# Performance work log

Hardware: AMD Instinct MI355X
Metric: run time of the kernel (lower is better)

The kernel has to match this reference:

```python
import jax, jax.numpy as jnp
import numpy as np

P_SZ = 16      # patch size
N_PATCH = 196  # (224/16)^2
D = 768        # feat dim (= 3*16*16)
H = 3072       # mlp hidden
T = 8          # num task vectors
P_BLOCKS = 6   # param blocks: Wp, bp, W1, b1, W2, b2
META_H = 192   # max(768//4, T*P_BLOCKS)


def patchify(x):
    # x: [B,3,224,224] -> [B,196,768]
    B = x.shape[0]
    x = x.reshape(B, 3, 14, P_SZ, 14, P_SZ)
    x = x.transpose(0, 2, 4, 1, 3, 5)
    return x.reshape(B, N_PATCH, 3 * P_SZ * P_SZ)


def func0(params, xp):
    # surrogate linearized backbone on ONE sample's patches xp: [196,768] -> [768]
    Wp, bp, W1, b1, W2, b2 = params
    h = xp @ Wp + bp              # [196,768]
    f = h.mean(axis=0)            # [768]
    f = jax.nn.relu(f @ W1 + b1)  # [3072]
    return f @ W2 + b2            # [768]


def setup_inputs() -> dict:
    key = jax.random.key(0)
    ks = jax.random.split(key, 20)
    B = 32
    d = {}
    d['x'] = jax.random.normal(ks[0], (B, 3, 224, 224), dtype=jnp.float32)
    # base params0 (6 blocks)
    d['Wp'] = jax.random.normal(ks[1], (D, D), dtype=jnp.float32) * 0.02
    d['bp'] = jnp.zeros((D,), dtype=jnp.float32)
    d['W1'] = jax.random.normal(ks[2], (D, H), dtype=jnp.float32) * 0.02
    d['b1'] = jnp.zeros((H,), dtype=jnp.float32)
    d['W2'] = jax.random.normal(ks[3], (H, D), dtype=jnp.float32) * 0.02
    d['b2'] = jnp.zeros((D,), dtype=jnp.float32)
    # T stacked task-vector deltas, one per param block
    d['dWp'] = jax.random.normal(ks[4], (T, D, D), dtype=jnp.float32) * 0.01
    d['dbp'] = jax.random.normal(ks[5], (T, D), dtype=jnp.float32) * 0.01
    d['dW1'] = jax.random.normal(ks[6], (T, D, H), dtype=jnp.float32) * 0.01
    d['db1'] = jax.random.normal(ks[7], (T, H), dtype=jnp.float32) * 0.01
    d['dW2'] = jax.random.normal(ks[8], (T, H, D), dtype=jnp.float32) * 0.01
    d['db2'] = jax.random.normal(ks[9], (T, D), dtype=jnp.float32) * 0.01
    # MetaNet (Linear-ReLU-Linear), blockwise output T*P_BLOCKS
    d['mW1'] = jax.random.normal(ks[10], (D, META_H), dtype=jnp.float32) * 0.01
    d['mb1'] = jax.random.normal(ks[11], (META_H,), dtype=jnp.float32) * 0.01
    d['mW2'] = jax.random.normal(ks[12], (META_H, T * P_BLOCKS), dtype=jnp.float32) * 0.02
    d['mb2'] = jnp.zeros((T * P_BLOCKS,), dtype=jnp.float32)
    return d


def reference(x, Wp, bp, W1, b1, W2, b2,
              dWp, dbp, dW1, db1, dW2, db2,
              mW1, mb1, mW2, mb2):
    params0 = (Wp, bp, W1, b1, W2, b2)
    patches = patchify(x)                                  # [B,196,768]
    # base features (no grad in original)
    base_feat = jax.lax.stop_gradient(jax.vmap(lambda xp: func0(params0, xp))(patches))  # [B,768]
    # blockwise coefficients [B, T, P_BLOCKS]
    coefs = (jax.nn.relu(base_feat @ mW1 + mb1) @ mW2 + mb2).reshape(-1, T, P_BLOCKS)
    # batched weighted sum over task vectors, per parameter block
    dWp_b = jnp.einsum('bt,tij->bij', coefs[:, :, 0], dWp)
    dbp_b = jnp.einsum('bt,tj->bj',  coefs[:, :, 1], dbp)
    dW1_b = jnp.einsum('bt,tij->bij', coefs[:, :, 2], dW1)
    db1_b = jnp.einsum('bt,tj->bj',  coefs[:, :, 3], db1)
    dW2_b = jnp.einsum('bt,tij->bij', coefs[:, :, 4], dW2)
    db2_b = jnp.einsum('bt,tj->bj',  coefs[:, :, 5], db2)

    def single(xp, dp):
        out, dout = jax.jvp(lambda p: func0(p, xp), (params0,), (dp,))
        return out + dout

    outputs = jax.vmap(single)(patches, (dWp_b, dbp_b, dW1_b, db1_b, dW2_b, db2_b))
    return outputs  # [B,768]
```

## Files before the change

### kernel.cpp

```cpp
#include <hip/hip_runtime.h>


__global__ void patch_partial_k(const float* __restrict__ x, float* __restrict__ part) {
    int blk = blockIdx.x;
    int i  = blk % 14;
    int ch = (blk / 14) % 3;
    int b  = blk / 42;
    int t  = threadIdx.x;
    int py = t >> 4, px = t & 15;
    const float* xp = x + (((size_t)(b*3 + ch))*224 + (size_t)(i*16 + py))*224 + px;
    float s = 0.f;
#pragma unroll
    for (int j = 0; j < 14; ++j) s += xp[j*16];
    part[(size_t)blk*256 + t] = s;
}

__global__ void patch_reduce_k(const float* __restrict__ part, float* __restrict__ xbarT) {
    int idx = blockIdx.x*256 + threadIdx.x;
    int b = idx / 768;
    int c = idx % 768;
    int ch = c >> 8, t = c & 255;
    const float* p = part + ((size_t)(b*42 + ch*14))*256 + t;
    float s = 0.f;
#pragma unroll
    for (int i = 0; i < 14; ++i) s += p[i*256];
    xbarT[(size_t)c*32 + b] = s * (1.f/196.f);
}

#define LOADB(BUF)                                                   \
    _Pragma("unroll")                                                \
    for (int u = 0; u < 16; ++u) BUF[u] = bp[(size_t)u*N];           \
    bp += (size_t)16*N;

#define FMAC8(AR, BV)                                                \
    _Pragma("unroll")                                                \
    for (int m = 0; m < 8; ++m) {                                    \
        acc[4*m]   += AR[m].x * (BV);                                \
        acc[4*m+1] += AR[m].y * (BV);                                \
        acc[4*m+2] += AR[m].z * (BV);                                \
        acc[4*m+3] += AR[m].w * (BV);                                \
    }

#define PREF(AR, KIDX)                                               \
    _Pragma("unroll")                                                \
    for (int r = 0; r < 8; ++r)                                      \
        AR[r] = *(const float4*)(As + (KIDX)*32 + r*4);

#define HALF(BUF, KK)                                                \
    _Pragma("unroll")                                                \
    for (int u = 0; u < 16; u += 2) {                                \
        PREF(a1, (KK)+u+1)                                           \
        FMAC8(a0, BUF[u])                                            \
        PREF(a0, (KK)+u+2)                                           \
        FMAC8(a1, BUF[u+1])                                          \
    }

template<int N, int KW>
__global__ __launch_bounds__(256, 3) void gemm4_k(const float* __restrict__ AT,
                                                  const float* __restrict__ Bm,
                                                  float* __restrict__ P) {
    constexpr int KB = 4*KW;
    __shared__ float lds[8704];
    const int tid  = threadIdx.x;
    const int lane = tid & 63;
    const int wave = __builtin_amdgcn_readfirstlane(tid >> 6);
    const int col  = blockIdx.x*64 + lane;
    const size_t kblk = (size_t)blockIdx.y * KB;

    {
        const float4* Ag = (const float4*)(AT + kblk*32);
        float4* As4 = (float4*)lds;
#pragma unroll
        for (int i = 0; i < KB*32/4/256; ++i)
            As4[i*256 + tid] = Ag[i*256 + tid];
    }

    const float* bp = Bm + (kblk + (size_t)wave*KW)*N + col;
    float bvA[16], bvB[16];
    LOADB(bvA)

    __syncthreads();
    const float* As = lds + wave*KW*32;

    float acc[32];
#pragma unroll
    for (int m = 0; m < 32; ++m) acc[m] = 0.f;

    float4 a0[8], a1[8];
    PREF(a0, 0)

    if constexpr (KW == 16) {
        HALF(bvA, 0)
    } else {
#pragma unroll 1
        for (int kk = 0; kk + 32 <= KW; kk += 32) {
            LOADB(bvB)
            HALF(bvA, kk)
            if (kk + 32 < KW) { LOADB(bvA) }
            HALF(bvB, kk + 16)
        }
    }

    __syncthreads();
    {
        float* w0 = lds + (wave*64 + lane)*34;
#pragma unroll
        for (int m = 0; m < 32; m += 2)
            *(float2*)(w0 + m) = make_float2(acc[m], acc[m+1]);
    }
    __syncthreads();
    {
        const int c  = tid >> 2;
        const int mb = (tid & 3) * 8;
        float s[8];
#pragma unroll
        for (int j = 0; j < 8; j += 2) {
            float2 v0 = *(const float2*)(lds + (0*64 + c)*34 + mb + j);
            float2 v1 = *(const float2*)(lds + (1*64 + c)*34 + mb + j);
            float2 v2 = *(const float2*)(lds + (2*64 + c)*34 + mb + j);
            float2 v3 = *(const float2*)(lds + (3*64 + c)*34 + mb + j);
            s[j]   = v0.x + v1.x + v2.x + v3.x;
            s[j+1] = v0.y + v1.y + v2.y + v3.y;
        }
        float* p0 = P + (size_t)blockIdx.y*((size_t)N*32)
                      + ((size_t)blockIdx.x*64 + c)*32 + mb;
        *(float4*)(p0)     = make_float4(s[0], s[1], s[2], s[3]);
        *(float4*)(p0 + 4) = make_float4(s[4], s[5], s[6], s[7]);
    }
}

template<int Y>
__global__ void reduce_bias_k(const float* __restrict__ P, const float* __restrict__ bias,
                              float* __restrict__ out, int SZ) {
    int idx = blockIdx.x*256 + threadIdx.x;
    float s = bias[idx >> 5];
#pragma unroll
    for (int y = 0; y < Y; ++y) s += P[(size_t)y*SZ + idx];
    out[idx] = s;
}

template<int Y>
__global__ void reduce_zf_k(const float* __restrict__ P, const float* __restrict__ bias,
                            float* __restrict__ zT, float* __restrict__ fT) {
    int idx = blockIdx.x*256 + threadIdx.x;
    float s = bias[idx >> 5];
#pragma unroll
    for (int y = 0; y < Y; ++y) s += P[(size_t)y*98304 + idx];
    zT[idx] = s;
    fT[idx] = fmaxf(s, 0.f);
}

template<int Y>
__global__ void reduce_arr_k(const float* __restrict__ P, const float* __restrict__ init,
                             float* __restrict__ out, int SZ) {
    int idx = blockIdx.x*256 + threadIdx.x;
    float s = init[idx];
#pragma unroll
    for (int y = 0; y < Y; ++y) s += P[(size_t)y*SZ + idx];
    out[idx] = s;
}

template<int Y>
__global__ void reduce_mask_k(const float* __restrict__ P, const float* __restrict__ init,
                              const float* __restrict__ zT, float* __restrict__ dfT) {
    int idx = blockIdx.x*256 + threadIdx.x;
    float s = init[idx];
#pragma unroll 15
    for (int y = 0; y < Y; ++y) s += P[(size_t)y*98304 + idx];
    dfT[idx] = zT[idx] > 0.f ? s : 0.f;
}

template<int Y>
__global__ void reduce_out_k(const float* __restrict__ P, const float* __restrict__ init,
                             const float* __restrict__ baseT, float* __restrict__ out) {
    int idx = blockIdx.x*256 + threadIdx.x;
    float s = init[idx] + baseT[idx];
#pragma unroll 15
    for (int y = 0; y < Y; ++y) s += P[(size_t)y*24576 + idx];
    int n = idx >> 5, b = idx & 31;
    out[b*768 + n] = s;
}

__global__ void metanet1_k(const float* __restrict__ baseT, const float* __restrict__ mW1,
                           const float* __restrict__ mb1, float* __restrict__ v) {
    int b  = blockIdx.x;
    int jg = blockIdx.y;
    int jj = threadIdx.x & 31;
    int ks = threadIdx.x >> 5;
    int j  = jg*32 + jj;
    const float* wp = mW1 + (size_t)(ks*96)*192 + j;
    const float* xp = baseT + (size_t)(ks*96)*32 + b;
    float s = 0.f;
#pragma unroll 8
    for (int i = 0; i < 96; ++i) s += xp[i*32] * wp[i*192];
    __shared__ float red[256];
    red[threadIdx.x] = s;
    __syncthreads();
    if (threadIdx.x < 32) {
        float t = mb1[j];
#pragma unroll
        for (int k = 0; k < 8; ++k) t += red[k*32 + threadIdx.x];
        v[b*192 + jg*32 + threadIdx.x] = fmaxf(t, 0.f);
    }
}

__global__ void metanet2_k(const float* __restrict__ v, const float* __restrict__ mW2,
                           const float* __restrict__ mb2, float* __restrict__ coefs) {
    int b  = blockIdx.x;
    int o  = threadIdx.x & 63;
    int ks = threadIdx.x >> 6;
    float s = 0.f;
    if (o < 48) {
        const float* vp = v + b*192 + ks*48;
        const float* wp = mW2 + (size_t)(ks*48)*48 + o;
#pragma unroll 8
        for (int i = 0; i < 48; ++i) s += vp[i] * wp[i*48];
    }
    __shared__ float red[256];
    red[threadIdx.x] = s;
    __syncthreads();
    if (threadIdx.x < 48) {
        float t = mb2[threadIdx.x];
#pragma unroll
        for (int k = 0; k < 4; ++k) t += red[k*64 + threadIdx.x];
        coefs[b*48 + threadIdx.x] = t;
    }
}

__global__ void build_all_k(const float* __restrict__ coefs, const float* __restrict__ xbarT,
                            const float* __restrict__ f0T, const float* __restrict__ fT,
                            const float* __restrict__ dbp, const float* __restrict__ db1,
                            const float* __restrict__ db2,
                            float* __restrict__ G0T, float* __restrict__ G1T,
                            float* __restrict__ G2T, float* __restrict__ df0b,
                            float* __restrict__ dzb, float* __restrict__ doutb) {
    int idx = blockIdx.x*256 + threadIdx.x;
    int b = idx & 31;
    int r = idx >> 5;
    if (r < 6144) {
        int t = r / 768, i = r % 768;
        G0T[idx] = coefs[b*48 + t*6 + 0] * xbarT[(size_t)i*32 + b];
    } else if (r < 12288) {
        int rr = r - 6144;
        int t = rr / 768, i = rr % 768;
        G1T[(size_t)rr*32 + b] = coefs[b*48 + t*6 + 2] * f0T[(size_t)i*32 + b];
    } else if (r < 36864) {
        int rr = r - 12288;
        int t = rr / 3072, i = rr % 3072;
        G2T[(size_t)rr*32 + b] = coefs[b*48 + t*6 + 4] * fT[(size_t)i*32 + b];
    } else if (r < 37632) {
        int n = r - 36864;
        float s = 0.f;
#pragma unroll
        for (int t = 0; t < 8; ++t) s += coefs[b*48 + t*6 + 1] * dbp[t*768 + n];
        df0b[(size_t)n*32 + b] = s;
    } else if (r < 40704) {
        int n = r - 37632;
        float s = 0.f;
#pragma unroll
        for (int t = 0; t < 8; ++t) s += coefs[b*48 + t*6 + 3] * db1[t*3072 + n];
        dzb[(size_t)n*32 + b] = s;
    } else if (r < 41472) {
        int n = r - 40704;
        float s = 0.f;
#pragma unroll
        for (int t = 0; t < 8; ++t) s += coefs[b*48 + t*6 + 5] * db2[t*768 + n];
        doutb[(size_t)n*32 + b] = s;
    }
}

extern "C" void kernel_launch(void* const* d_in, const int* in_sizes, int n_in,
                              void* d_out, int out_size, void* d_ws, size_t ws_size,
                              hipStream_t stream) {
    const float* x   = (const float*)d_in[0];
    const float* Wp  = (const float*)d_in[1];
    const float* bp  = (const float*)d_in[2];
    const float* W1  = (const float*)d_in[3];
    const float* b1  = (const float*)d_in[4];
    const float* W2  = (const float*)d_in[5];
    const float* b2  = (const float*)d_in[6];
    const float* dWp = (const float*)d_in[7];
    const float* dbp = (const float*)d_in[8];
    const float* dW1 = (const float*)d_in[9];
    const float* db1 = (const float*)d_in[10];
    const float* dW2 = (const float*)d_in[11];
    const float* db2 = (const float*)d_in[12];
    const float* mW1 = (const float*)d_in[13];
    const float* mb1 = (const float*)d_in[14];
    const float* mW2 = (const float*)d_in[15];
    const float* mb2 = (const float*)d_in[16];
    float* out = (float*)d_out;

    float* ws    = (float*)d_ws;
    float* part  = ws;
    float* xbarT = part  + 344064;
    float* f0T   = xbarT + 24576;
    float* zT    = f0T   + 24576;
    float* fT    = zT    + 98304;
    float* baseT = fT    + 98304;
    float* coefs = baseT + 24576;
    float* G0T   = coefs + 1536;
    float* G1T   = G0T   + 196608;
    float* G2T   = G1T   + 196608;
    float* df0b  = G2T   + 786432;
    float* dzb   = df0b  + 24576;
    float* doutb = dzb   + 98304;
    float* dfT   = doutb + 24576;
    float* df0T  = dfT   + 98304;
    float* A1 = df0T + 24576;
    float* A2 = A1 + 3145728;
    float* A3 = A2 + 3145728;
    float* mv = A3 + 1179648;

    patch_partial_k<<<1344, 256, 0, stream>>>(x, part);
    patch_reduce_k<<<96, 256, 0, stream>>>(part, xbarT);

    gemm4_k<768, 16><<<dim3(12, 12), 256, 0, stream>>>(xbarT, Wp, A3);
    reduce_bias_k<12><<<96, 256, 0, stream>>>(A3, bp, f0T, 24576);
    gemm4_k<3072, 16><<<dim3(48, 12), 256, 0, stream>>>(f0T, W1, A1);
    reduce_zf_k<12><<<384, 256, 0, stream>>>(A1, b1, zT, fT);
    gemm4_k<768, 16><<<dim3(12, 48), 256, 0, stream>>>(fT, W2, A2);
    reduce_bias_k<48><<<96, 256, 0, stream>>>(A2, b2, baseT, 24576);

    metanet1_k<<<dim3(32, 6), 256, 0, stream>>>(baseT, mW1, mb1, mv);
    metanet2_k<<<32, 256, 0, stream>>>(mv, mW2, mb2, coefs);

    build_all_k<<<5184, 256, 0, stream>>>(coefs, xbarT, f0T, fT, dbp, db1, db2,
                                          G0T, G1T, G2T, df0b, dzb, doutb);

    gemm4_k<768, 32><<<dim3(12, 48), 256, 0, stream>>>(G0T, dWp, A3);
    reduce_arr_k<48><<<96, 256, 0, stream>>>(A3, df0b, df0T, 24576);
    gemm4_k<3072, 32><<<dim3(48, 6), 256, 0, stream>>>(df0T, W1, A1);
    gemm4_k<3072, 64><<<dim3(48, 24), 256, 0, stream>>>(G1T, dW1, A1 + (size_t)6*98304);
    reduce_mask_k<30><<<384, 256, 0, stream>>>(A1, dzb, zT, dfT);
    gemm4_k<768, 32><<<dim3(12, 24), 256, 0, stream>>>(dfT, W2, A2);
    gemm4_k<768, 64><<<dim3(12, 96), 256, 0, stream>>>(G2T, dW2, A2 + (size_t)24*24576);
    reduce_out_k<120><<<96, 256, 0, stream>>>(A2, doutb, baseT, out);
}
```

Measured before the change: 337.1 us.

## Widen GEMM tiles to 128 columns per block and rebalance split-K

Each thread now computes two 64-column halves, so every LDS load of the A fragment feeds twice as many FMAs and the grid halves in the column dimension. Launch bounds drop to 2 blocks per SM to fit the doubled accumulators, and the split-K factors change (more K slices, shorter per-block K, new KW=48 path), with workspace and reduction kernels resized to match. This trades occupancy and more partial-sum traffic for better register-level data reuse in the weight-streaming GEMMs.

```diff
diff --git a/kernel.cpp b/kernel.cpp
--- a/kernel.cpp
+++ b/kernel.cpp
@@ -27,18 +27,25 @@
     xbarT[(size_t)c*32 + b] = s * (1.f/196.f);
 }
 
-#define LOADB(BUF)                                                   \
+#define LOADB2(BV, BW)                                               \
     _Pragma("unroll")                                                \
-    for (int u = 0; u < 16; ++u) BUF[u] = bp[(size_t)u*N];           \
+    for (int u = 0; u < 16; ++u) {                                   \
+        BV[u] = bp[(size_t)u*N];                                     \
+        BW[u] = bp[(size_t)u*N + 64];                                 \
+    }                                                                \
     bp += (size_t)16*N;
 
-#define FMAC8(AR, BV)                                                \
+#define FMAC8x2(AR, BVU, BWU)                                        \
     _Pragma("unroll")                                                \
     for (int m = 0; m < 8; ++m) {                                    \
-        acc[4*m]   += AR[m].x * (BV);                                \
-        acc[4*m+1] += AR[m].y * (BV);                                \
-        acc[4*m+2] += AR[m].z * (BV);                                \
-        acc[4*m+3] += AR[m].w * (BV);                                \
+        acc0[4*m]   += AR[m].x * (BVU);                              \
+        acc0[4*m+1] += AR[m].y * (BVU);                              \
+        acc0[4*m+2] += AR[m].z * (BVU);                              \
+        acc0[4*m+3] += AR[m].w * (BVU);                              \
+        acc1[4*m]   += AR[m].x * (BWU);                              \
+        acc1[4*m+1] += AR[m].y * (BWU);                              \
+        acc1[4*m+2] += AR[m].z * (BWU);                              \
+        acc1[4*m+3] += AR[m].w * (BWU);                              \
     }
 
 #define PREF(AR, KIDX)                                               \
@@ -46,17 +53,17 @@
     for (int r = 0; r < 8; ++r)                                      \
         AR[r] = *(const float4*)(As + (KIDX)*32 + r*4);
 
-#define HALF(BUF, KK)                                                \
+#define HALF2(BV, BW, KK)                                            \
     _Pragma("unroll")                                                \
     for (int u = 0; u < 16; u += 2) {                                \
         PREF(a1, (KK)+u+1)                                           \
-        FMAC8(a0, BUF[u])                                            \
+        FMAC8x2(a0, BV[u], BW[u])                                    \
         PREF(a0, (KK)+u+2)                                           \
-        FMAC8(a1, BUF[u+1])                                          \
+        FMAC8x2(a1, BV[u+1], BW[u+1])                                \
     }
 
 template<int N, int KW>
-__global__ __launch_bounds__(256, 3) void gemm4_k(const float* __restrict__ AT,
+__global__ __launch_bounds__(256, 2) void gemm5_k(const float* __restrict__ AT,
                                                   const float* __restrict__ Bm,
                                                   float* __restrict__ P) {
     constexpr int KB = 4*KW;
@@ -64,54 +71,65 @@
     const int tid  = threadIdx.x;
     const int lane = tid & 63;
     const int wave = __builtin_amdgcn_readfirstlane(tid >> 6);
-    const int col  = blockIdx.x*64 + lane;
     const size_t kblk = (size_t)blockIdx.y * KB;
 
     {
         const float4* Ag = (const float4*)(AT + kblk*32);
         float4* As4 = (float4*)lds;
 #pragma unroll
-        for (int i = 0; i < KB*32/4/256; ++i)
+        for (int i = 0; i < KB*32/1024; ++i)
             As4[i*256 + tid] = Ag[i*256 + tid];
     }
 
-    const float* bp = Bm + (kblk + (size_t)wave*KW)*N + col;
-    float bvA[16], bvB[16];
-    LOADB(bvA)
+    const float* bp = Bm + (kblk + (size_t)wave*KW)*N + blockIdx.x*128 + lane;
+    float bvA[16], bwA[16], bvB[16], bwB[16];
+    LOADB2(bvA, bwA)
 
     __syncthreads();
     const float* As = lds + wave*KW*32;
 
-    float acc[32];
-#pragma unroll
-    for (int m = 0; m < 32; ++m) acc[m] = 0.f;
+    float acc0[32], acc1[32];
+#pragma unroll
+    for (int m = 0; m < 32; ++m) { acc0[m] = 0.f; acc1[m] = 0.f; }
 
     float4 a0[8], a1[8];
     PREF(a0, 0)
 
     if constexpr (KW == 16) {
-        HALF(bvA, 0)
+        HALF2(bvA, bwA, 0)
+    } else if constexpr (KW % 32 == 0) {
+#pragma unroll 1
+        for (int kk = 0; kk + 64 <= KW; kk += 32) {
+            LOADB2(bvB, bwB)
+            HALF2(bvA, bwA, kk)
+            LOADB2(bvA, bwA)
+            HALF2(bvB, bwB, kk + 16)
+        }
+        LOADB2(bvB, bwB)
+        HALF2(bvA, bwA, KW - 32)
+        HALF2(bvB, bwB, KW - 16)
     } else {
 #pragma unroll 1
-        for (int kk = 0; kk + 32 <= KW; kk += 32) {
-            LOADB(bvB)
-            HALF(bvA, kk)
-            if (kk + 32 < KW) { LOADB(bvA) }
-            HALF(bvB, kk + 16)
+        for (int kk = 0; kk + 48 <= KW; kk += 32) {
+            LOADB2(bvB, bwB)
+            HALF2(bvA, bwA, kk)
+            LOADB2(bvA, bwA)
+            HALF2(bvB, bwB, kk + 16)
         }
-    }
-
-    __syncthreads();
+        HALF2(bvA, bwA, KW - 16)
+    }
+
+    __syncthreads();
+    const int c  = tid >> 2;
+    const int mb = (tid & 3) * 8;
     {
         float* w0 = lds + (wave*64 + lane)*34;
 #pragma unroll
         for (int m = 0; m < 32; m += 2)
-            *(float2*)(w0 + m) = make_float2(acc[m], acc[m+1]);
-    }
-    __syncthreads();
-    {
-        const int c  = tid >> 2;
-        const int mb = (tid & 3) * 8;
+            *(float2*)(w0 + m) = make_float2(acc0[m], acc0[m+1]);
+    }
+    __syncthreads();
+    {
         float s[8];
 #pragma unroll
         for (int j = 0; j < 8; j += 2) {
@@ -123,7 +141,31 @@
             s[j+1] = v0.y + v1.y + v2.y + v3.y;
         }
         float* p0 = P + (size_t)blockIdx.y*((size_t)N*32)
-                      + ((size_t)blockIdx.x*64 + c)*32 + mb;
+                      + ((size_t)blockIdx.x*128 + c)*32 + mb;
+        *(float4*)(p0)     = make_float4(s[0], s[1], s[2], s[3]);
+        *(float4*)(p0 + 4) = make_float4(s[4], s[5], s[6], s[7]);
+    }
+    __syncthreads();
+    {
+        float* w0 = lds + (wave*64 + lane)*34;
+#pragma unroll
+        for (int m = 0; m < 32; m += 2)
+            *(float2*)(w0 + m) = make_float2(acc1[m], acc1[m+1]);
+    }
+    __syncthreads();
+    {
+        float s[8];
+#pragma unroll
+        for (int j = 0; j < 8; j += 2) {
+            float2 v0 = *(const float2*)(lds + (0*64 + c)*34 + mb + j);
+            float2 v1 = *(const float2*)(lds + (1*64 + c)*34 + mb + j);
+            float2 v2 = *(const float2*)(lds + (2*64 + c)*34 + mb + j);
+            float2 v3 = *(const float2*)(lds + (3*64 + c)*34 + mb + j);
+            s[j]   = v0.x + v1.x + v2.x + v3.x;
+            s[j+1] = v0.y + v1.y + v2.y + v3.y;
+        }
+        float* p0 = P + (size_t)blockIdx.y*((size_t)N*32)
+                      + ((size_t)blockIdx.x*128 + 64 + c)*32 + mb;
         *(float4*)(p0)     = make_float4(s[0], s[1], s[2], s[3]);
         *(float4*)(p0 + 4) = make_float4(s[4], s[5], s[6], s[7]);
     }
@@ -155,7 +197,7 @@
                              float* __restrict__ out, int SZ) {
     int idx = blockIdx.x*256 + threadIdx.x;
     float s = init[idx];
-#pragma unroll
+#pragma unroll 16
     for (int y = 0; y < Y; ++y) s += P[(size_t)y*SZ + idx];
     out[idx] = s;
 }
@@ -165,7 +207,7 @@
                               const float* __restrict__ zT, float* __restrict__ dfT) {
     int idx = blockIdx.x*256 + threadIdx.x;
     float s = init[idx];
-#pragma unroll 15
+#pragma unroll 16
     for (int y = 0; y < Y; ++y) s += P[(size_t)y*98304 + idx];
     dfT[idx] = zT[idx] > 0.f ? s : 0.f;
 }
@@ -175,7 +217,7 @@
                              const float* __restrict__ baseT, float* __restrict__ out) {
     int idx = blockIdx.x*256 + threadIdx.x;
     float s = init[idx] + baseT[idx];
-#pragma unroll 15
+#pragma unroll 16
     for (int y = 0; y < Y; ++y) s += P[(size_t)y*24576 + idx];
     int n = idx >> 5, b = idx & 31;
     out[b*768 + n] = s;
@@ -307,19 +349,19 @@
     float* doutb = dzb   + 98304;
     float* dfT   = doutb + 24576;
     float* df0T  = dfT   + 98304;
-    float* A1 = df0T + 24576;
-    float* A2 = A1 + 3145728;
-    float* A3 = A2 + 3145728;
-    float* mv = A3 + 1179648;
+    float* mv    = df0T  + 24576;
+    float* A1 = mv + 6144;
+    float* A2 = A1 + (size_t)44*98304;
+    float* A3 = A2 + (size_t)176*24576;
 
     patch_partial_k<<<1344, 256, 0, stream>>>(x, part);
     patch_reduce_k<<<96, 256, 0, stream>>>(part, xbarT);
 
-    gemm4_k<768, 16><<<dim3(12, 12), 256, 0, stream>>>(xbarT, Wp, A3);
+    gemm5_k<768, 16><<<dim3(6, 12), 256, 0, stream>>>(xbarT, Wp, A3);
     reduce_bias_k<12><<<96, 256, 0, stream>>>(A3, bp, f0T, 24576);
-    gemm4_k<3072, 16><<<dim3(48, 12), 256, 0, stream>>>(f0T, W1, A1);
+    gemm5_k<3072, 16><<<dim3(24, 12), 256, 0, stream>>>(f0T, W1, A1);
     reduce_zf_k<12><<<384, 256, 0, stream>>>(A1, b1, zT, fT);
-    gemm4_k<768, 16><<<dim3(12, 48), 256, 0, stream>>>(fT, W2, A2);
+    gemm5_k<768, 16><<<dim3(6, 48), 256, 0, stream>>>(fT, W2, A2);
     reduce_bias_k<48><<<96, 256, 0, stream>>>(A2, b2, baseT, 24576);
 
     metanet1_k<<<dim3(32, 6), 256, 0, stream>>>(baseT, mW1, mb1, mv);
@@ -328,12 +370,12 @@
     build_all_k<<<5184, 256, 0, stream>>>(coefs, xbarT, f0T, fT, dbp, db1, db2,
                                           G0T, G1T, G2T, df0b, dzb, doutb);
 
-    gemm4_k<768, 32><<<dim3(12, 48), 256, 0, stream>>>(G0T, dWp, A3);
-    reduce_arr_k<48><<<96, 256, 0, stream>>>(A3, df0b, df0T, 24576);
-    gemm4_k<3072, 32><<<dim3(48, 6), 256, 0, stream>>>(df0T, W1, A1);
-    gemm4_k<3072, 64><<<dim3(48, 24), 256, 0, stream>>>(G1T, dW1, A1 + (size_t)6*98304);
-    reduce_mask_k<30><<<384, 256, 0, stream>>>(A1, dzb, zT, dfT);
-    gemm4_k<768, 32><<<dim3(12, 24), 256, 0, stream>>>(dfT, W2, A2);
-    gemm4_k<768, 64><<<dim3(12, 96), 256, 0, stream>>>(G2T, dW2, A2 + (size_t)24*24576);
-    reduce_out_k<120><<<96, 256, 0, stream>>>(A2, doutb, baseT, out);
-}
+    gemm5_k<768, 16><<<dim3(6, 96), 256, 0, stream>>>(G0T, dWp, A3);
+    reduce_arr_k<96><<<96, 256, 0, stream>>>(A3, df0b, df0T, 24576);
+    gemm5_k<3072, 16><<<dim3(24, 12), 256, 0, stream>>>(df0T, W1, A1);
+    gemm5_k<3072, 48><<<dim3(24, 32), 256, 0, stream>>>(G1T, dW1, A1 + (size_t)12*98304);
+    reduce_mask_k<44><<<384, 256, 0, stream>>>(A1, dzb, zT, dfT);
+    gemm5_k<768, 16><<<dim3(6, 48), 256, 0, stream>>>(dfT, W2, A2);
+    gemm5_k<768, 48><<<dim3(6, 128), 256, 0, stream>>>(G2T, dW2, A2 + (size_t)48*24576);
+    reduce_out_k<176><<<96, 256, 0, stream>>>(A2, doutb, baseT, out);
+}
```

Result: slower. 607.7 us (+80.3%).
